# Kernel optimization log

Measured on AMD Instinct MI355X. Metric: run time of the kernel, lower is better.

The kernel has to match this reference:

```python
import jax, jax.numpy as jnp
import numpy as np

N = 30000      # nodes
E = 480000     # edges
H = 128        # hidden_nf
NQ = 7         # qubits
D = 2 ** NQ    # 128, quantum state dim == embedding_size
NL = 2         # block n_layers (QGCL layers)
QL = 2         # quantum circuit layers inside each QGCL
NORM = 100.0   # normalization_factor ('sum' aggregation)
NORM_CONST = 1.0


def _cnot_perm_indices(n):
    # Composed permutation for CNOT(0,1)...CNOT(n-2,n-1), CNOT(n-1,0).
    # PennyLane convention: wire 0 is the most significant bit.
    idx = np.arange(2 ** n)
    pairs = [(i, i + 1) for i in range(n - 1)] + [(n - 1, 0)]
    g = None
    for c, t in pairs:
        cb = (idx >> (n - 1 - c)) & 1
        f = idx ^ (cb << (n - 1 - t))  # flip target bit if control set (involution)
        g = f if g is None else g[f]
    return g

_CNOT_G = jnp.asarray(_cnot_perm_indices(NQ))


def _quantum_states(q_in, coeffs, A_re, A_im):
    """Vectorized VQC over all nodes. q_in [N,D] real -> [N,D] complex state."""
    norm = jnp.sqrt(jnp.sum(q_in ** 2, axis=1, keepdims=True) + 1e-12)
    s = (q_in / norm).astype(jnp.complex64)  # normalized initial state per node
    I = jnp.eye(D, dtype=jnp.complex64)
    for j in range(QL):
        # Cayley transform -> unitary
        A = (A_re[j] + 1j * A_im[j]).astype(jnp.complex64)
        A = A + A.conj().T
        q = (A - 1j * I) @ jnp.linalg.inv(A + 1j * I)
        # single-qubit layer: RY(b) @ RX(a) on every qubit -> kron power
        a, b = coeffs[j, 0].astype(jnp.complex64), coeffs[j, 1].astype(jnp.complex64)
        ca, sa = jnp.cos(a / 2), jnp.sin(a / 2)
        cb, sb = jnp.cos(b / 2), jnp.sin(b / 2)
        RX = jnp.stack([jnp.stack([ca, -1j * sa]), jnp.stack([-1j * sa, ca])])
        RY = jnp.stack([jnp.stack([cb, -sb]), jnp.stack([sb, cb])])
        G = RY @ RX
        Gk = G
        for _ in range(NQ - 1):
            Gk = jnp.kron(Gk, G)
        s = s @ q.T            # QubitUnitary
        s = s @ Gk.T           # RX/RY on all qubits
        s = s[:, _CNOT_G]      # CNOT ring (pure permutation)
    return s


def setup_inputs() -> dict:
    key = jax.random.key(0)
    ks = jax.random.split(key, 20)
    return {
        "h": jax.random.normal(ks[0], (N, H), jnp.float32),
        "x": jax.random.normal(ks[1], (N, 3), jnp.float32),
        "edge_index": jax.random.randint(ks[2], (2, E), 0, N, jnp.int32),
        "edge_attr": jax.random.normal(ks[3], (E, 1), jnp.float32),
        "e_w1": jax.random.normal(ks[4], (NL, 2 * H + 2, H), jnp.float32) * 0.05,
        "e_b1": jnp.zeros((NL, H), jnp.float32),
        "e_w2": jax.random.normal(ks[5], (NL, H, H), jnp.float32) * 0.05,
        "e_b2": jnp.zeros((NL, H), jnp.float32),
        "enc_w": jax.random.normal(ks[6], (NL, 2 * H, D), jnp.float32) * 0.05,
        "enc_b": jnp.zeros((NL, D), jnp.float32),
        "coeffs": jax.random.normal(ks[7], (NL, QL, 2), jnp.float32) * 0.1,
        "A_re": jax.random.normal(ks[8], (NL, QL, D, D), jnp.float32) * 0.01,
        "A_im": jax.random.normal(ks[9], (NL, QL, D, D), jnp.float32) * 0.01,
        "dec_w": jax.random.normal(ks[10], (NL, D, H), jnp.float32) * 0.05,
        "dec_b": jnp.zeros((NL, H), jnp.float32),
        "c_w1": jax.random.normal(ks[11], (2 * H + 2, H), jnp.float32) * 0.05,
        "c_b1": jnp.zeros((H,), jnp.float32),
        "c_w2": jax.random.normal(ks[12], (H, H), jnp.float32) * 0.05,
        "c_b2": jnp.zeros((H,), jnp.float32),
        "c_w3": jax.random.normal(ks[13], (H, 1), jnp.float32) * 0.001,  # xavier gain=0.001
    }


def reference(h, x, edge_index, edge_attr, e_w1, e_b1, e_w2, e_b2, enc_w, enc_b,
              coeffs, A_re, A_im, dec_w, dec_b, c_w1, c_b1, c_w2, c_b2, c_w3):
    row, col = edge_index[0], edge_index[1]
    # coord2diff
    diff = x[row] - x[col]
    radial = jnp.sum(diff ** 2, axis=1, keepdims=True)     # [E,1] (used as 'distances')
    coord_diff = diff / (jnp.sqrt(radial + 1e-8) + NORM_CONST)
    eattr = jnp.concatenate([radial, edge_attr], axis=1)   # [E,2]

    for l in range(NL):  # QGCL layers
        m = jnp.concatenate([h[row], h[col], eattr], axis=1)       # [E, 2H+2]
        m = jax.nn.silu(m @ e_w1[l] + e_b1[l])
        m = jax.nn.silu(m @ e_w2[l] + e_b2[l])                     # edge messages mij
        agg = jax.ops.segment_sum(m, row, num_segments=N) / NORM   # scatter-add
        q_in = jnp.concatenate([h, agg], axis=1) @ enc_w[l] + enc_b[l]
        # quantum part is detached in the original (torch .detach + re-tensor)
        qs = jax.lax.stop_gradient(
            _quantum_states(q_in, coeffs[l], A_re[l], A_im[l]))
        h = h + qs.real.astype(h.dtype) @ dec_w[l] + dec_b[l]

    # EquivariantUpdate (tanh=False)
    t = jnp.concatenate([h[row], h[col], eattr], axis=1)
    t = jax.nn.silu(t @ c_w1 + c_b1)
    t = jax.nn.silu(t @ c_w2 + c_b2)
    t = t @ c_w3                                                   # [E,1]
    trans = coord_diff * t
    x = x + jax.ops.segment_sum(trans, row, num_segments=N) / NORM
    return h, x
```

## Files before the change

### kernel.cpp

```cpp
#include <hip/hip_runtime.h>
#include <math.h>

#define N_NODES 30000
#define N_EDGES 480000
#define HDIM 128
#define EPB 64
#define NAS 264
#define MS 136
#define M2TS 72

typedef __attribute__((ext_vector_type(8))) short short8b;
typedef __attribute__((ext_vector_type(4))) float f32x4;

__device__ __forceinline__ float silu_f(float v) {
  return v / (1.0f + __expf(-v));
}

__device__ __forceinline__ unsigned short f2bf(float f) {
  unsigned int u = __float_as_uint(f);
  unsigned int r = u + 0x7fffu + ((u >> 16) & 1u);
  return (unsigned short)(r >> 16);
}

__device__ __forceinline__ unsigned int cvt_pk_bf16(float lo, float hi) {
  unsigned int r;
  asm("v_cvt_pk_bf16_f32 %0, %1, %2" : "=v"(r) : "v"(lo), "v"(hi));
  return r;
}

__device__ __forceinline__ ushort4 pk4(float4 v) {
  uint2 u;
  u.x = cvt_pk_bf16(v.x, v.y);
  u.y = cvt_pk_bf16(v.z, v.w);
  return *(ushort4*)&u;
}

__global__ void init_out_bf_kernel(const float* __restrict__ h,
                                   const float* __restrict__ x,
                                   const int* __restrict__ ei,
                                   float* __restrict__ out,
                                   int* __restrict__ cursor) {
  int idx = blockIdx.x * 256 + threadIdx.x;
  ((float4*)out)[idx] = ((const float4*)h)[idx];
  if (idx < N_NODES * 3 / 4) {
    ((float4*)(out + N_NODES * HDIM))[idx] = ((const float4*)x)[idx];
  }
  if (idx < N_EDGES) atomicAdd(&cursor[ei[idx]], 1);
}

__global__ __launch_bounds__(1024) void scan_kernel(int* __restrict__ cursor,
                                                    int* __restrict__ cstart) {
  __shared__ int sums[1024];
  const int tid = threadIdx.x;
  const int base = tid * 30;
  int local[30];
  int s = 0;
#pragma unroll
  for (int j = 0; j < 30; ++j) {
    int idx = base + j;
    int d = (idx < N_NODES) ? cursor[idx] : 0;
    local[j] = s;
    s += d;
  }
  sums[tid] = s;
  __syncthreads();
  for (int off = 1; off < 1024; off <<= 1) {
    int add = (tid >= off) ? sums[tid - off] : 0;
    __syncthreads();
    sums[tid] += add;
    __syncthreads();
  }
  int excl = (tid == 0) ? 0 : sums[tid - 1];
#pragma unroll
  for (int j = 0; j < 30; ++j) {
    int idx = base + j;
    if (idx < N_NODES) {
      int v = excl + local[j];
      cursor[idx] = v;
      cstart[idx] = v;
    }
  }
}

__global__ void prep_kernel(
    const int* __restrict__ ei, int* __restrict__ cursor,
    unsigned int* __restrict__ rcp, float2* __restrict__ era,
    const float* __restrict__ x, const float* __restrict__ ea,
    const float* __restrict__ e_w1, const float* __restrict__ e_w2,
    const float* __restrict__ enc_w, const float* __restrict__ c_w1,
    const float* __restrict__ c_w2,
    ushort* __restrict__ w1cs, ushort* __restrict__ w2cs,
    ushort* __restrict__ enccs, ushort* __restrict__ cw1cs,
    ushort* __restrict__ cw2cs,
    const float* __restrict__ A_re, const float* __restrict__ A_im,
    float2* __restrict__ X,
    const float* __restrict__ coeffs, float2* __restrict__ gkm,
    const float* __restrict__ outh, const float* __restrict__ b1l0,
    ushort* __restrict__ P) {
  __shared__ ushort Ht[EPB * MS];
  const int b = blockIdx.x, tid = threadIdx.x;
  if (b < 1875) {
    int e = b * 256 + tid;
    int r = ei[e];
    int c = ei[N_EDGES + e];
    int pos = atomicAdd(&cursor[r], 1);
    rcp[pos] = (unsigned int)r | ((unsigned int)c << 16);
    float dx = x[r * 3 + 0] - x[c * 3 + 0];
    float dy = x[r * 3 + 1] - x[c * 3 + 1];
    float dz = x[r * 3 + 2] - x[c * 3 + 2];
    era[pos] = make_float2(dx * dx + dy * dy + dz * dz, ea[e]);
  } else if (b < 2755) {
    int idx = (b - 1875) * 256 + tid;
    int ci = idx >> 12, rem = idx & 4095, kk = rem & 31;
    const float* W; ushort* dst; int Kreal, ktl;
    if (ci < 18) {
      int l = ci / 9; ktl = ci - l * 9;
      W = e_w1 + (size_t)l * 258 * HDIM; dst = w1cs + (size_t)l * 9 * 4096;
      Kreal = 258;
    } else if (ci < 26) {
      int c2 = ci - 18; int l = c2 >> 2; ktl = c2 & 3;
      W = e_w2 + (size_t)l * HDIM * HDIM; dst = w2cs + (size_t)l * 4 * 4096;
      Kreal = 128;
    } else if (ci < 42) {
      int c2 = ci - 26; int l = c2 >> 3; ktl = c2 & 7;
      W = enc_w + (size_t)l * 256 * HDIM; dst = enccs + (size_t)l * 8 * 4096;
      Kreal = 256;
    } else if (ci < 51) {
      ktl = ci - 42; W = c_w1; dst = cw1cs; Kreal = 258;
    } else {
      ktl = ci - 51; W = c_w2; dst = cw2cs; Kreal = 128;
    }
    int n = rem >> 5;
    int k = ktl * 32 + kk;
    float v = (k < Kreal) ? W[(size_t)k * HDIM + n] : 0.0f;
    dst[ktl * 4096 + rem] = f2bf(v);
  } else if (b < 3011) {
    int bb = b - 2755;
    int lj = bb >> 6;
    int idx = (bb & 63) * 256 + tid;
    int r = idx >> 7, c = idx & 127;
    const float* are = A_re + (size_t)lj * 16384;
    const float* aim = A_im + (size_t)lj * 16384;
    float re = are[r * 128 + c] + are[c * 128 + r];
    float im = aim[r * 128 + c] - aim[c * 128 + r];
    if (r == c) im -= 1.0f;
    X[(size_t)lj * 16384 + idx] = make_float2(re, im);
  } else if (b < 3267) {
    int bb = b - 3011;
    int lj = bb >> 6;
    float a = coeffs[lj * 2 + 0], bcf = coeffs[lj * 2 + 1];
    float ca = cosf(0.5f * a), sa = sinf(0.5f * a);
    float cb = cosf(0.5f * bcf), sb = sinf(0.5f * bcf);
    float2 G[2][2];
    G[0][0] = make_float2(cb * ca, sb * sa);
    G[0][1] = make_float2(-sb * ca, -cb * sa);
    G[1][0] = make_float2(sb * ca, -cb * sa);
    G[1][1] = make_float2(cb * ca, -sb * sa);
    int idx = (bb & 63) * 256 + tid;
    int r = idx >> 7, c = idx & 127;
    float2 acc = make_float2(1.f, 0.f);
#pragma unroll
    for (int bit = 6; bit >= 0; --bit) {
      float2 g = G[(r >> bit) & 1][(c >> bit) & 1];
      acc = make_float2(acc.x * g.x - acc.y * g.y, acc.x * g.y + acc.y * g.x);
    }
    gkm[(size_t)lj * 16384 + idx] = acc;
  } else {
    const int n0 = (b - 3267) * EPB;
    const int lane = tid & 63, wave = tid >> 6;
    const int lrow = lane & 15, lq = lane >> 4;
    {
      const int e = tid >> 2, jj = tid & 3;
      int node = n0 + e;
      if (node >= N_NODES) node = N_NODES - 1;
      const float4* s4 = (const float4*)(outh + (size_t)node * HDIM + jj * 32);
      ushort* dst = Ht + e * MS + jj * 32;
#pragma unroll
      for (int i = 0; i < 8; ++i) {
        ((ushort4*)dst)[i] = pk4(s4[i]);
      }
    }
    short8b wf[4][4];
    const int cs = (wave >> 1) * 4;
    const int nb = (wave & 1) * 64;
#pragma unroll
    for (int kt = 0; kt < 4; ++kt)
#pragma unroll
      for (int nt = 0; nt < 4; ++nt)
        wf[kt][nt] = *(const short8b*)(w1cs + (cs + kt) * 4096 + (nb + nt * 16 + lrow) * 32 + lq * 8);
    __syncthreads();

    f32x4 acc[4][4];
#pragma unroll
    for (int mt = 0; mt < 4; ++mt)
#pragma unroll
      for (int nt = 0; nt < 4; ++nt) acc[mt][nt] = (f32x4){0.f, 0.f, 0.f, 0.f};
#pragma unroll
    for (int kt = 0; kt < 4; ++kt) {
      short8b af[4];
#pragma unroll
      for (int mt = 0; mt < 4; ++mt)
        af[mt] = *(const short8b*)(Ht + (mt * 16 + lrow) * MS + kt * 32 + lq * 8);
#pragma unroll
      for (int mt = 0; mt < 4; ++mt)
#pragma unroll
        for (int nt = 0; nt < 4; ++nt)
          acc[mt][nt] = __builtin_amdgcn_mfma_f32_16x16x32_bf16(af[mt], wf[kt][nt], acc[mt][nt], 0, 0, 0);
    }
    const int cbase = wave * 64;
#pragma unroll
    for (int nt = 0; nt < 4; ++nt) {
      const int ccol = cbase + nt * 16 + lrow;
      const float bb2 = (ccol < 128) ? b1l0[ccol] : 0.f;
#pragma unroll
      for (int mt = 0; mt < 4; ++mt)
#pragma unroll
        for (int r = 0; r < 4; ++r) {
          const int node = n0 + mt * 16 + lq * 4 + r;
          if (node < N_NODES) P[(size_t)node * 256 + ccol] = f2bf(acc[mt][nt][r] + bb2);
        }
    }
  }
}

__global__ void ns_bx_kernel(const float* __restrict__ Are,
                             const float* __restrict__ Aim,
                             const float2* __restrict__ X,
                             float2* __restrict__ T) {
  int lj = blockIdx.y;
  int idx = blockIdx.x * 256 + threadIdx.x;
  int r = idx >> 7, c = idx & 127;
  const float* are = Are + (size_t)lj * 16384;
  const float* aim = Aim + (size_t)lj * 16384;
  const float2* x = X + (size_t)lj * 16384;
  float2 acc = make_float2(0.f, 0.f);
  for (int k = 0; k < 128; ++k) {
    float re = are[r * 128 + k] + are[k * 128 + r];
    float im = aim[r * 128 + k] - aim[k * 128 + r];
    if (k == r) im += 1.0f;
    float2 b = x[k * 128 + c];
    acc.x += re * b.x - im * b.y;
    acc.y += re * b.y + im * b.x;
  }
  T[(size_t)lj * 16384 + idx] = acc;
}

__global__ void ns_upd_kernel(const float2* __restrict__ X,
                              const float2* __restrict__ T,
                              float2* __restrict__ Xn) {
  int lj = blockIdx.y;
  int idx = blockIdx.x * 256 + threadIdx.x;
  int r = idx >> 7, c = idx & 127;
  const float2* x = X + (size_t)lj * 16384;
  const float2* t = T + (size_t)lj * 16384;
  float2 acc = make_float2(0.f, 0.f);
  for (int k = 0; k < 128; ++k) {
    float2 a = x[r * 128 + k];
    float2 b = t[k * 128 + c];
    acc.x += a.x * b.x - a.y * b.y;
    acc.y += a.x * b.y + a.y * b.x;
  }
  float2 xc = x[r * 128 + c];
  Xn[(size_t)lj * 16384 + idx] = make_float2(2.f * xc.x - acc.x, 2.f * xc.y - acc.y);
}

__global__ void qmat_kernel(const float* __restrict__ Are,
                            const float* __restrict__ Aim,
                            const float2* __restrict__ binvg,
                            float2* __restrict__ qm) {
  int lj = blockIdx.y;
  int idx = blockIdx.x * 256 + threadIdx.x;
  int r = idx >> 7, c = idx & 127;
  const float* are = Are + (size_t)lj * 16384;
  const float* aim = Aim + (size_t)lj * 16384;
  const float2* binv = binvg + (size_t)lj * 16384;
  float2 acc = make_float2(0.f, 0.f);
  for (int k = 0; k < 128; ++k) {
    float re = are[r * 128 + k] + are[k * 128 + r];
    float im = aim[r * 128 + k] - aim[k * 128 + r];
    if (k == r) im -= 1.0f;
    float2 b = binv[k * 128 + c];
    acc.x += re * b.x - im * b.y;
    acc.y += re * b.y + im * b.x;
  }
  qm[(size_t)lj * 16384 + idx] = acc;
}

__global__ void nj_kernel(const float2* __restrict__ qm,
                          const float2* __restrict__ gkm,
                          float2* __restrict__ njm) {
  int lj = blockIdx.y;
  int idx = blockIdx.x * 256 + threadIdx.x;
  int i = idx >> 7, c = idx & 127;
  int gc;
  {
    int v = c;
    const int cs[7] = {6, 5, 4, 3, 2, 1, 0};
    const int ts[7] = {0, 6, 5, 4, 3, 2, 1};
#pragma unroll
    for (int p = 0; p < 7; ++p) {
      int cb = (v >> (6 - cs[p])) & 1;
      v = v ^ (cb << (6 - ts[p]));
    }
    gc = v;
  }
  const float2* q = qm + (size_t)lj * 16384;
  const float2* gk = gkm + (size_t)lj * 16384;
  float2 acc = make_float2(0.f, 0.f);
  for (int k = 0; k < 128; ++k) {
    float2 qa = q[k * 128 + i];
    float2 gb = gk[gc * 128 + k];
    acc.x += qa.x * gb.x - qa.y * gb.y;
    acc.y += qa.x * gb.y + qa.y * gb.x;
  }
  njm[(size_t)lj * 16384 + idx] = acc;
}

__global__ void compose_kernel(const float2* __restrict__ njm,
                               float2* __restrict__ um) {
  int l = blockIdx.y;
  int idx = blockIdx.x * 256 + threadIdx.x;
  int i = idx >> 7, c = idx & 127;
  const float2* n0 = njm + (size_t)(l * 2 + 0) * 16384;
  const float2* n1 = njm + (size_t)(l * 2 + 1) * 16384;
  float2 acc = make_float2(0.f, 0.f);
  for (int k = 0; k < 128; ++k) {
    float2 a = n0[i * 128 + k];
    float2 b = n1[k * 128 + c];
    acc.x += a.x * b.x - a.y * b.y;
    acc.y += a.x * b.y + a.y * b.x;
  }
  um[(size_t)l * 16384 + idx] = acc;
}

__global__ void wqd_kernel(const float2* __restrict__ um,
                           const float* __restrict__ decw,
                           ushort* __restrict__ wqdcs) {
  int l = blockIdx.y;
  int idx = blockIdx.x * 256 + threadIdx.x;
  int i = idx >> 7, c = idx & 127;
  const float2* u = um + (size_t)l * 16384;
  const float* dw = decw + (size_t)l * 16384;
  float acc = 0.f;
  for (int k = 0; k < 128; ++k) acc += u[i * 128 + k].x * dw[k * 128 + c];
  wqdcs[(size_t)l * 4 * 4096 + (i >> 5) * 4096 + c * 32 + (i & 31)] = f2bf(acc);
}

__global__ __launch_bounds__(256, 4) void edge_mfma_kernel(
    const ushort* __restrict__ P, const unsigned int* __restrict__ rcp,
    const float2* __restrict__ era, const int* __restrict__ cstart,
    const float* __restrict__ wm,
    const ushort* __restrict__ w2cs, const float* __restrict__ b2,
    float* __restrict__ agg, float* __restrict__ headp) {
  __shared__ ushort buf[128 * M2TS];
  __shared__ int rows[EPB];
  __shared__ __align__(16) ushort segv[EPB];
  __shared__ int segnode[EPB];
  __shared__ int scont, snseg;
  ushort* m1 = buf;
  ushort* m2t = buf;

  const int tid = threadIdx.x;
  const int lane = tid & 63, wave = tid >> 6;
  const int lrow = lane & 15, lq = lane >> 4;
  const int wbase = wave * 32;
  const int woff0 = (wbase + lrow) * 32 + lq * 8;
  const int woff1 = (wbase + 16 + lrow) * 32 + lq * 8;
  const float b2v[2] = {b2[wbase + lrow], b2[wbase + 16 + lrow]};

  const int i0 = blockIdx.x * EPB;
  {
    const int e = tid >> 2, j = tid & 3;
    const unsigned int rcv = rcp[i0 + e];
    const int r = (int)(rcv & 0xFFFFu), c = (int)(rcv >> 16);
    if (j == 0) rows[e] = r;
    const float2 re2 = era[i0 + e];
    const float radial = re2.x, eav = re2.y;
    const uint4* pr = (const uint4*)(P + (size_t)r * 256 + j * 32);
    const uint4* pc = (const uint4*)(P + (size_t)c * 256 + 128 + j * 32);
    uint4 PR[4] = {pr[0], pr[1], pr[2], pr[3]};
    uint4 PC[4] = {pc[0], pc[1], pc[2], pc[3]};
#pragma unroll
    for (int q = 0; q < 4; ++q) {
      const int kb = j * 32 + q * 8;
      const uint ua[4] = {PR[q].x, PR[q].y, PR[q].z, PR[q].w};
      const uint ub[4] = {PC[q].x, PC[q].y, PC[q].z, PC[q].w};
      uint ow[4];
#pragma unroll
      for (int w = 0; w < 4; ++w) {
        const int k = kb + w * 2;
        float v0 = __uint_as_float(ua[w] << 16) + __uint_as_float(ub[w] << 16)
                 + radial * wm[k] + eav * wm[128 + k];
        float v1 = __uint_as_float(ua[w] & 0xffff0000u) + __uint_as_float(ub[w] & 0xffff0000u)
                 + radial * wm[k + 1] + eav * wm[129 + k];
        ow[w] = cvt_pk_bf16(silu_f(v0), silu_f(v1));
      }
      uint4 o; o.x = ow[0]; o.y = ow[1]; o.z = ow[2]; o.w = ow[3];
      *(uint4*)(m1 + e * MS + kb) = o;
    }
  }
  __syncthreads();

  f32x4 acc2[4][2];
#pragma unroll
  for (int mt = 0; mt < 4; ++mt)
#pragma unroll
    for (int nt = 0; nt < 2; ++nt) acc2[mt][nt] = (f32x4){0.f, 0.f, 0.f, 0.f};
  {
    short8b wcur0 = *(const short8b*)(w2cs + woff0);
    short8b wcur1 = *(const short8b*)(w2cs + woff1);
#pragma unroll
    for (int kt = 0; kt < 4; ++kt) {
      short8b wn0, wn1;
      if (kt < 3) {
        wn0 = *(const short8b*)(w2cs + (kt + 1) * 4096 + woff0);
        wn1 = *(const short8b*)(w2cs + (kt + 1) * 4096 + woff1);
      }
      short8b af[4];
#pragma unroll
      for (int mt = 0; mt < 4; ++mt)
        af[mt] = *(const short8b*)(m1 + (mt * 16 + lrow) * MS + kt * 32 + lq * 8);
#pragma unroll
      for (int mt = 0; mt < 4; ++mt) {
        acc2[mt][0] = __builtin_amdgcn_mfma_f32_16x16x32_bf16(af[mt], wcur0, acc2[mt][0], 0, 0, 0);
        acc2[mt][1] = __builtin_amdgcn_mfma_f32_16x16x32_bf16(af[mt], wcur1, acc2[mt][1], 0, 0, 0);
      }
      if (kt < 3) { wcur0 = wn0; wcur1 = wn1; }
    }
  }
  __syncthreads();

#pragma unroll
  for (int mt = 0; mt < 4; ++mt)
#pragma unroll
    for (int nt = 0; nt < 2; ++nt) {
      const int col = wbase + nt * 16 + lrow;
      uint2 u;
      u.x = cvt_pk_bf16(silu_f(acc2[mt][nt][0] + b2v[nt]),
                        silu_f(acc2[mt][nt][1] + b2v[nt]));
      u.y = cvt_pk_bf16(silu_f(acc2[mt][nt][2] + b2v[nt]),
                        silu_f(acc2[mt][nt][3] + b2v[nt]));
      *(uint2*)(m2t + col * M2TS + mt * 16 + lq * 4) = u;
    }
  if (wave == 0) {
    const int e = lane;
    const int re_ = rows[e];
    const bool leader = (e == 0) || (rows[e - 1] != re_);
    const unsigned long long mask = __ballot(leader);
    const int seg = (int)__popcll(mask & ((1ull << e) - 1ull));
    segv[e] = (ushort)seg;
    if (leader) segnode[seg] = re_;
    if (e == 0) {
      snseg = (int)__popcll(mask);
      scont = (cstart[re_] < i0) ? 1 : 0;
    }
  }
  __syncthreads();

  const int nseg = snseg, cont = scont;
  const int ntmax = (nseg + 15) >> 4;
  const short8b sv0 = *(const short8b*)(segv + lq * 8);
  const short8b sv1 = *(const short8b*)(segv + 32 + lq * 8);
  const int mtb = wave * 32;
  short8b afr[2][2];
#pragma unroll
  for (int mt = 0; mt < 2; ++mt) {
    const ushort* rp = m2t + (mtb + mt * 16 + lrow) * M2TS + lq * 8;
    afr[mt][0] = *(const short8b*)(rp);
    afr[mt][1] = *(const short8b*)(rp + 32);
  }
  for (int nt = 0; nt < ntmax; ++nt) {
    const int tgt = nt * 16 + lrow;
    uint p0[4], p1[4];
#pragma unroll
    for (int w = 0; w < 4; ++w) {
      p0[w] = (((int)(ushort)sv0[2 * w] == tgt) ? 0x3F80u : 0u)
            | (((int)(ushort)sv0[2 * w + 1] == tgt) ? 0x3F800000u : 0u);
      p1[w] = (((int)(ushort)sv1[2 * w] == tgt) ? 0x3F80u : 0u)
            | (((int)(ushort)sv1[2 * w + 1] == tgt) ? 0x3F800000u : 0u);
    }
    uint4 u0 = make_uint4(p0[0], p0[1], p0[2], p0[3]);
    uint4 u1 = make_uint4(p1[0], p1[1], p1[2], p1[3]);
    const short8b bf0 = *(const short8b*)&u0;
    const short8b bf1 = *(const short8b*)&u1;
    f32x4 r0 = (f32x4){0.f, 0.f, 0.f, 0.f};
    f32x4 r1 = (f32x4){0.f, 0.f, 0.f, 0.f};
    r0 = __builtin_amdgcn_mfma_f32_16x16x32_bf16(afr[0][0], bf0, r0, 0, 0, 0);
    r0 = __builtin_amdgcn_mfma_f32_16x16x32_bf16(afr[0][1], bf1, r0, 0, 0, 0);
    r1 = __builtin_amdgcn_mfma_f32_16x16x32_bf16(afr[1][0], bf0, r1, 0, 0, 0);
    r1 = __builtin_amdgcn_mfma_f32_16x16x32_bf16(afr[1][1], bf1, r1, 0, 0, 0);
    const int seg = tgt;
    if (seg < nseg) {
      const int node = segnode[seg];
      float* dst = (seg == 0 && cont) ? (headp + (size_t)blockIdx.x * HDIM)
                                      : (agg + (size_t)node * HDIM);
#pragma unroll
      for (int r = 0; r < 4; ++r) {
        dst[mtb + lq * 4 + r] = r0[r];
        dst[mtb + 16 + lq * 4 + r] = r1[r];
      }
    }
  }
}

__global__ __launch_bounds__(256, 2) void node_mfma_kernel(
    float* __restrict__ out_h, const float* __restrict__ agg,
    const int* __restrict__ cstart, const int* __restrict__ cend,
    const float* __restrict__ headp,
    const ushort* __restrict__ enccs, const float* __restrict__ encb,
    const ushort* __restrict__ wqdcs, const float* __restrict__ decb,
    const ushort* __restrict__ w1n, const float* __restrict__ b1n,
    ushort* __restrict__ Pout) {
  __shared__ ushort A[EPB * NAS];
  __shared__ ushort m1[EPB * MS];
  __shared__ float nbuf[4 * EPB];
  const int tid = threadIdx.x;
  const int n0 = blockIdx.x * EPB;

  const int lane = tid & 63, wave = tid >> 6;
  const int lrow = lane & 15, lq = lane >> 4;
  const int wbase = wave * 32;

  short8b wef[8][2], wqf[4][2];
#pragma unroll
  for (int kt = 0; kt < 8; ++kt)
#pragma unroll
    for (int nt = 0; nt < 2; ++nt)
      wef[kt][nt] = *(const short8b*)(enccs + kt * 4096 + (wbase + nt * 16 + lrow) * 32 + lq * 8);
#pragma unroll
  for (int kt = 0; kt < 4; ++kt)
#pragma unroll
    for (int nt = 0; nt < 2; ++nt)
      wqf[kt][nt] = *(const short8b*)(wqdcs + kt * 4096 + (wbase + nt * 16 + lrow) * 32 + lq * 8);
  const float ebv[2] = {encb[wbase + lrow], encb[wbase + 16 + lrow]};
  const float dbv[2] = {decb[wbase + lrow], decb[wbase + 16 + lrow]};

  {
    const int e = tid >> 2, j = tid & 3;
    int node = n0 + e;
    if (node >= N_NODES) node = N_NODES - 1;
    if (j < 2) {
      const float4* s4 = (const float4*)(out_h + (size_t)node * HDIM + j * 64);
      ushort* dst = A + e * NAS + j * 64;
#pragma unroll
      for (int i = 0; i < 16; ++i) {
        ((ushort4*)dst)[i] = pk4(s4[i]);
      }
    } else {
      const int s = cstart[node], en = cend[node];
      const bool hasAgg = en > s;
      const float4* a4 = (const float4*)(agg + (size_t)node * HDIM + (j - 2) * 64);
      const int bb0 = (s >> 6) + 1;
      const int bb1 = hasAgg ? ((en - 1) >> 6) : 0;
      ushort* dst = A + e * NAS + 128 + (j - 2) * 64;
#pragma unroll
      for (int i = 0; i < 16; ++i) {
        float4 v = hasAgg ? a4[i] : make_float4(0.f, 0.f, 0.f, 0.f);
        for (int bb = bb0; bb <= bb1; ++bb) {
          float4 hv = *(const float4*)(headp + (size_t)bb * HDIM + (j - 2) * 64 + i * 4);
          v.x += hv.x; v.y += hv.y; v.z += hv.z; v.w += hv.w;
        }
        float4 sv = make_float4(v.x * 0.01f, v.y * 0.01f, v.z * 0.01f, v.w * 0.01f);
        ((ushort4*)dst)[i] = pk4(sv);
      }
    }
  }
  __syncthreads();

  f32x4 acc[4][2];
#pragma unroll
  for (int mt = 0; mt < 4; ++mt)
#pragma unroll
    for (int nt = 0; nt < 2; ++nt) acc[mt][nt] = (f32x4){0.f, 0.f, 0.f, 0.f};
#pragma unroll
  for (int kt = 0; kt < 8; ++kt) {
    short8b af[4];
#pragma unroll
    for (int mt = 0; mt < 4; ++mt)
      af[mt] = *(const short8b*)(A + (mt * 16 + lrow) * NAS + kt * 32 + lq * 8);
#pragma unroll
    for (int mt = 0; mt < 4; ++mt)
#pragma unroll
      for (int nt = 0; nt < 2; ++nt)
        acc[mt][nt] = __builtin_amdgcn_mfma_f32_16x16x32_bf16(af[mt], wef[kt][nt], acc[mt][nt], 0, 0, 0);
  }
#pragma unroll
  for (int mt = 0; mt < 4; ++mt) {
    float ssp[4] = {0.f, 0.f, 0.f, 0.f};
#pragma unroll
    for (int nt = 0; nt < 2; ++nt)
#pragma unroll
      for (int r = 0; r < 4; ++r) {
        acc[mt][nt][r] += ebv[nt];
        ssp[r] += acc[mt][nt][r] * acc[mt][nt][r];
      }
#pragma unroll
    for (int m = 1; m < 16; m <<= 1)
#pragma unroll
      for (int r = 0; r < 4; ++r) ssp[r] += __shfl_xor(ssp[r], m, 64);
    if (lrow == 0) {
#pragma unroll
      for (int r = 0; r < 4; ++r)
        nbuf[wave * EPB + mt * 16 + lq * 4 + r] = ssp[r];
    }
  }
  __syncthreads();
#pragma unroll
  for (int mt = 0; mt < 4; ++mt)
#pragma unroll
    for (int r = 0; r < 4; ++r) {
      const int row = mt * 16 + lq * 4 + r;
      float sum = nbuf[row] + nbuf[EPB + row] + nbuf[2 * EPB + row] + nbuf[3 * EPB + row];
      float inv = 1.0f / sqrtf(sum + 1e-12f);
#pragma unroll
      for (int nt = 0; nt < 2; ++nt)
        m1[row * MS + wbase + nt * 16 + lrow] = f2bf(acc[mt][nt][r] * inv);
    }
  __syncthreads();

  f32x4 acc2[4][2];
#pragma unroll
  for (int mt = 0; mt < 4; ++mt)
#pragma unroll
    for (int nt = 0; nt < 2; ++nt) acc2[mt][nt] = (f32x4){0.f, 0.f, 0.f, 0.f};
#pragma unroll
  for (int kt = 0; kt < 4; ++kt) {
    short8b af[4];
#pragma unroll
    for (int mt = 0; mt < 4; ++mt)
      af[mt] = *(const short8b*)(m1 + (mt * 16 + lrow) * MS + kt * 32 + lq * 8);
#pragma unroll
    for (int mt = 0; mt < 4; ++mt)
#pragma unroll
      for (int nt = 0; nt < 2; ++nt)
        acc2[mt][nt] = __builtin_amdgcn_mfma_f32_16x16x32_bf16(af[mt], wqf[kt][nt], acc2[mt][nt], 0, 0, 0);
  }
  __syncthreads();

#pragma unroll
  for (int mt = 0; mt < 4; ++mt)
#pragma unroll
    for (int nt = 0; nt < 2; ++nt) {
      const int n = wbase + nt * 16 + lrow;
#pragma unroll
      for (int r = 0; r < 4; ++r) {
        const int node = n0 + mt * 16 + lq * 4 + r;
        float hn = 0.f;
        if (node < N_NODES) {
          size_t off = (size_t)node * HDIM + n;
          hn = out_h[off] + acc2[mt][nt][r] + dbv[nt];
          out_h[off] = hn;
        }
        m1[(mt * 16 + lq * 4 + r) * MS + n] = f2bf(hn);
      }
    }
  __syncthreads();

  short8b wfp[4][4];
  const int csn = (wave >> 1) * 4;
  const int nbw = (wave & 1) * 64;
#pragma unroll
  for (int kt = 0; kt < 4; ++kt)
#pragma unroll
    for (int nt = 0; nt < 4; ++nt)
      wfp[kt][nt] = *(const short8b*)(w1n + (csn + kt) * 4096 + (nbw + nt * 16 + lrow) * 32 + lq * 8);
  f32x4 pacc[4][4];
#pragma unroll
  for (int mt = 0; mt < 4; ++mt)
#pragma unroll
    for (int nt = 0; nt < 4; ++nt) pacc[mt][nt] = (f32x4){0.f, 0.f, 0.f, 0.f};
#pragma unroll
  for (int kt = 0; kt < 4; ++kt) {
    short8b af[4];
#pragma unroll
    for (int mt = 0; mt < 4; ++mt)
      af[mt] = *(const short8b*)(m1 + (mt * 16 + lrow) * MS + kt * 32 + lq * 8);
#pragma unroll
    for (int mt = 0; mt < 4; ++mt)
#pragma unroll
      for (int nt = 0; nt < 4; ++nt)
        pacc[mt][nt] = __builtin_amdgcn_mfma_f32_16x16x32_bf16(af[mt], wfp[kt][nt], pacc[mt][nt], 0, 0, 0);
  }
  const int cbase = wave * 64;
#pragma unroll
  for (int nt = 0; nt < 4; ++nt) {
    const int ccol = cbase + nt * 16 + lrow;
    const float bb2 = (ccol < 128) ? b1n[ccol] : 0.f;
#pragma unroll
    for (int mt = 0; mt < 4; ++mt)
#pragma unroll
      for (int r = 0; r < 4; ++r) {
        const int node = n0 + mt * 16 + lq * 4 + r;
        if (node < N_NODES) Pout[(size_t)node * 256 + ccol] = f2bf(pacc[mt][nt][r] + bb2);
      }
  }
}

__global__ __launch_bounds__(256, 4) void coord_mfma_kernel(
    const ushort* __restrict__ P, const unsigned int* __restrict__ rcp,
    const float2* __restrict__ era, const float* __restrict__ x,
    const float* __restrict__ wm,
    const ushort* __restrict__ w2cs, const float* __restrict__ b2,
    const float* __restrict__ w3, float* __restrict__ xout) {
  __shared__ ushort m1[EPB * MS];
  __shared__ int rows[EPB];
  __shared__ float pbuf[4 * EPB];
  __shared__ float tv[EPB];
  __shared__ float dxs[EPB], dys[EPB], dzs[EPB], ses[EPB];

  const int tid = threadIdx.x;
  const int lane = tid & 63, wave = tid >> 6;
  const int lrow = lane & 15, lq = lane >> 4;
  const int wbase = wave * 32;
  const int woff0 = (wbase + lrow) * 32 + lq * 8;
  const int woff1 = (wbase + 16 + lrow) * 32 + lq * 8;

  const float b2v[2] = {b2[wbase + lrow], b2[wbase + 16 + lrow]};
  const float w3v[2] = {w3[wbase + lrow], w3[wbase + 16 + lrow]};

  const int i0 = blockIdx.x * EPB;
  {
    const int e = tid >> 2, j = tid & 3;
    const unsigned int rcv = rcp[i0 + e];
    const int r = (int)(rcv & 0xFFFFu), c = (int)(rcv >> 16);
    if (j == 0) rows[e] = r;
    const float2 re2 = era[i0 + e];
    const float radial = re2.x, eav = re2.y;
    const uint4* pr = (const uint4*)(P + (size_t)r * 256 + j * 32);
    const uint4* pc = (const uint4*)(P + (size_t)c * 256 + 128 + j * 32);
    uint4 PR[4] = {pr[0], pr[1], pr[2], pr[3]};
    uint4 PC[4] = {pc[0], pc[1], pc[2], pc[3]};
    if (j == 3) {
      float dx = x[r * 3 + 0] - x[c * 3 + 0];
      float dy = x[r * 3 + 1] - x[c * 3 + 1];
      float dz = x[r * 3 + 2] - x[c * 3 + 2];
      dxs[e] = dx; dys[e] = dy; dzs[e] = dz;
      ses[e] = 1.0f / (sqrtf(radial + 1e-8f) + 1.0f);
    }
#pragma unroll
    for (int q = 0; q < 4; ++q) {
      const int kb = j * 32 + q * 8;
      const uint ua[4] = {PR[q].x, PR[q].y, PR[q].z, PR[q].w};
      const uint ub[4] = {PC[q].x, PC[q].y, PC[q].z, PC[q].w};
      uint ow[4];
#pragma unroll
      for (int w = 0; w < 4; ++w) {
        const int k = kb + w * 2;
        float v0 = __uint_as_float(ua[w] << 16) + __uint_as_float(ub[w] << 16)
                 + radial * wm[k] + eav * wm[128 + k];
        float v1 = __uint_as_float(ua[w] & 0xffff0000u) + __uint_as_float(ub[w] & 0xffff0000u)
                 + radial * wm[k + 1] + eav * wm[129 + k];
        ow[w] = cvt_pk_bf16(silu_f(v0), silu_f(v1));
      }
      uint4 o; o.x = ow[0]; o.y = ow[1]; o.z = ow[2]; o.w = ow[3];
      *(uint4*)(m1 + e * MS + kb) = o;
    }
  }
  __syncthreads();

  f32x4 acc2[4][2];
#pragma unroll
  for (int mt = 0; mt < 4; ++mt)
#pragma unroll
    for (int nt = 0; nt < 2; ++nt) acc2[mt][nt] = (f32x4){0.f, 0.f, 0.f, 0.f};
  {
    short8b wcur0 = *(const short8b*)(w2cs + woff0);
    short8b wcur1 = *(const short8b*)(w2cs + woff1);
#pragma unroll
    for (int kt = 0; kt < 4; ++kt) {
      short8b wn0, wn1;
      if (kt < 3) {
        wn0 = *(const short8b*)(w2cs + (kt + 1) * 4096 + woff0);
        wn1 = *(const short8b*)(w2cs + (kt + 1) * 4096 + woff1);
      }
      short8b af[4];
#pragma unroll
      for (int mt = 0; mt < 4; ++mt)
        af[mt] = *(const short8b*)(m1 + (mt * 16 + lrow) * MS + kt * 32 + lq * 8);
#pragma unroll
      for (int mt = 0; mt < 4; ++mt) {
        acc2[mt][0] = __builtin_amdgcn_mfma_f32_16x16x32_bf16(af[mt], wcur0, acc2[mt][0], 0, 0, 0);
        acc2[mt][1] = __builtin_amdgcn_mfma_f32_16x16x32_bf16(af[mt], wcur1, acc2[mt][1], 0, 0, 0);
      }
      if (kt < 3) { wcur0 = wn0; wcur1 = wn1; }
    }
  }
#pragma unroll
  for (int mt = 0; mt < 4; ++mt) {
    float p[4] = {0.f, 0.f, 0.f, 0.f};
#pragma unroll
    for (int nt = 0; nt < 2; ++nt)
#pragma unroll
      for (int r = 0; r < 4; ++r)
        p[r] += silu_f(acc2[mt][nt][r] + b2v[nt]) * w3v[nt];
#pragma unroll
    for (int m = 1; m < 16; m <<= 1)
#pragma unroll
      for (int r = 0; r < 4; ++r) p[r] += __shfl_xor(p[r], m, 64);
    if (lrow == 0) {
#pragma unroll
      for (int r = 0; r < 4; ++r)
        pbuf[wave * EPB + mt * 16 + lq * 4 + r] = p[r];
    }
  }
  __syncthreads();
  if (tid < EPB) {
    tv[tid] = (pbuf[tid] + pbuf[EPB + tid] + pbuf[2 * EPB + tid] + pbuf[3 * EPB + tid])
              * 0.01f * ses[tid];
  }
  __syncthreads();
  if (tid < EPB) {
    const int e = tid;
    const int r_e = rows[e];
    const bool leader = (e == 0) || (rows[e - 1] != r_e);
    if (leader) {
      float sx = 0.f, sy = 0.f, sz = 0.f;
      int f = e;
      do {
        float t = tv[f];
        sx += dxs[f] * t; sy += dys[f] * t; sz += dzs[f] * t;
        ++f;
      } while (f < EPB && rows[f] == r_e);
      atomicAdd(&xout[r_e * 3 + 0], sx);
      atomicAdd(&xout[r_e * 3 + 1], sy);
      atomicAdd(&xout[r_e * 3 + 2], sz);
    }
  }
}

extern "C" void kernel_launch(void* const* d_in, const int* in_sizes, int n_in,
                              void* d_out, int out_size, void* d_ws, size_t ws_size,
                              hipStream_t stream) {
  const float* h     = (const float*)d_in[0];
  const float* x     = (const float*)d_in[1];
  const int*   ei    = (const int*)d_in[2];
  const float* ea    = (const float*)d_in[3];
  const float* e_w1  = (const float*)d_in[4];
  const float* e_b1  = (const float*)d_in[5];
  const float* e_w2  = (const float*)d_in[6];
  const float* e_b2  = (const float*)d_in[7];
  const float* enc_w = (const float*)d_in[8];
  const float* enc_b = (const float*)d_in[9];
  const float* coeffs= (const float*)d_in[10];
  const float* A_re  = (const float*)d_in[11];
  const float* A_im  = (const float*)d_in[12];
  const float* dec_w = (const float*)d_in[13];
  const float* dec_b = (const float*)d_in[14];
  const float* c_w1  = (const float*)d_in[15];
  const float* c_b1  = (const float*)d_in[16];
  const float* c_w2  = (const float*)d_in[17];
  const float* c_b2  = (const float*)d_in[18];
  const float* c_w3  = (const float*)d_in[19];

  float* out = (float*)d_out;
  float* ws  = (float*)d_ws;

  float*        agg    = ws;
  float2*       xa     = (float2*)(ws + 3840000);
  float2*       xb     = (float2*)(ws + 3971072);
  float2*       xt     = (float2*)(ws + 4102144);
  float2*       qm     = (float2*)(ws + 4233216);
  float2*       gkm    = (float2*)(ws + 4364288);
  float2*       njm    = (float2*)(ws + 4495360);
  float2*       um     = (float2*)(ws + 4626432);
  int*          cursor = (int*)(ws + 4724864);
  int*          cstart = (int*)(ws + 4754864);
  unsigned int* rcp    = (unsigned int*)(ws + 4784864);
  float2*       era    = (float2*)(ws + 5264864);
  float*        headp  = ws + 6224864;
  ushort*       w1cs   = (ushort*)(ws + 7184864);
  ushort*       w2cs   = (ushort*)(ws + 7221728);
  ushort*       cw1cs  = (ushort*)(ws + 7238112);
  ushort*       cw2cs  = (ushort*)(ws + 7256544);
  ushort*       enccs  = (ushort*)(ws + 7264736);
  ushort*       wqdcs  = (ushort*)(ws + 7297504);
  ushort*       Pbuf   = (ushort*)(ws + 7313888);

  hipMemsetAsync(cursor, 0, N_NODES * sizeof(int), stream);
  init_out_bf_kernel<<<3750, 256, 0, stream>>>(h, x, ei, out, cursor);
  scan_kernel<<<1, 1024, 0, stream>>>(cursor, cstart);

  prep_kernel<<<3736, 256, 0, stream>>>(ei, cursor, rcp, era, x, ea,
                                        e_w1, e_w2, enc_w, c_w1, c_w2,
                                        w1cs, w2cs, enccs, cw1cs, cw2cs,
                                        A_re, A_im, xa, coeffs, gkm,
                                        out, e_b1, Pbuf);

  float2* cur = xa;
  float2* nxt = xb;
  for (int it = 0; it < 2; ++it) {
    ns_bx_kernel<<<dim3(64, 4), 256, 0, stream>>>(A_re, A_im, cur, xt);
    ns_upd_kernel<<<dim3(64, 4), 256, 0, stream>>>(cur, xt, nxt);
    float2* tmp = cur; cur = nxt; nxt = tmp;
  }
  qmat_kernel<<<dim3(64, 4), 256, 0, stream>>>(A_re, A_im, cur, qm);
  nj_kernel<<<dim3(64, 4), 256, 0, stream>>>(qm, gkm, njm);
  compose_kernel<<<dim3(64, 2), 256, 0, stream>>>(njm, um);
  wqd_kernel<<<dim3(64, 2), 256, 0, stream>>>(um, dec_w, wqdcs);

  const int NB = (N_NODES + EPB - 1) / EPB;

  for (int l = 0; l < 2; ++l) {
    edge_mfma_kernel<<<N_EDGES / EPB, 256, 0, stream>>>(
        Pbuf, rcp, era, cstart,
        e_w1 + (size_t)l * 258 * HDIM + 256 * HDIM,
        w2cs + (size_t)l * 4 * 4096, e_b2 + l * HDIM, agg, headp);
    node_mfma_kernel<<<NB, 256, 0, stream>>>(
        out, agg, cstart, cursor, headp,
        enccs + (size_t)l * 8 * 4096, enc_b + l * HDIM,
        wqdcs + (size_t)l * 4 * 4096, dec_b + l * HDIM,
        (l == 0) ? (w1cs + (size_t)9 * 4096) : cw1cs,
        (l == 0) ? (e_b1 + HDIM) : c_b1,
        Pbuf);
  }

  coord_mfma_kernel<<<N_EDGES / EPB, 256, 0, stream>>>(
      Pbuf, rcp, era, x, c_w1 + 256 * HDIM, cw2cs, c_b2, c_w3,
      out + (size_t)N_NODES * HDIM);
}
```

Baseline: 661.8 us.

## Halve edge tile to 32 edges with 128-thread blocks in edge and coord kernels

Edge-block size for the edge-message and coordinate kernels drops from 64 to 32 edges, and the blocks shrink to two waves. Each wave now computes 64 output columns over all 32 edges, and the segment-reduction MFMA is reworked for a single 32-edge K-slice. Head-partial indexing in the node kernel is updated to the new block size, and the workspace offsets move to fit the larger headp buffer. The aim is more resident blocks and less LDS per block, at the cost of twice as many blocks, more boundary partials, and reloading the weight fragments per block.

```diff
diff --git a/kernel.cpp b/kernel.cpp
--- a/kernel.cpp
+++ b/kernel.cpp
@@ -5,9 +5,10 @@
 #define N_EDGES 480000
 #define HDIM 128
 #define EPB 64
+#define EB 32
 #define NAS 264
 #define MS 136
-#define M2TS 72
+#define M2TS 36
 
 typedef __attribute__((ext_vector_type(8))) short short8b;
 typedef __attribute__((ext_vector_type(4))) float f32x4;
@@ -346,16 +347,16 @@
   wqdcs[(size_t)l * 4 * 4096 + (i >> 5) * 4096 + c * 32 + (i & 31)] = f2bf(acc);
 }
 
-__global__ __launch_bounds__(256, 4) void edge_mfma_kernel(
+__global__ __launch_bounds__(128, 8) void edge_mfma_kernel(
     const ushort* __restrict__ P, const unsigned int* __restrict__ rcp,
     const float2* __restrict__ era, const int* __restrict__ cstart,
     const float* __restrict__ wm,
     const ushort* __restrict__ w2cs, const float* __restrict__ b2,
     float* __restrict__ agg, float* __restrict__ headp) {
   __shared__ ushort buf[128 * M2TS];
-  __shared__ int rows[EPB];
-  __shared__ __align__(16) ushort segv[EPB];
-  __shared__ int segnode[EPB];
+  __shared__ int rows[EB];
+  __shared__ __align__(16) ushort segv[EB];
+  __shared__ int segnode[EB];
   __shared__ int scont, snseg;
   ushort* m1 = buf;
   ushort* m2t = buf;
@@ -363,12 +364,11 @@
   const int tid = threadIdx.x;
   const int lane = tid & 63, wave = tid >> 6;
   const int lrow = lane & 15, lq = lane >> 4;
-  const int wbase = wave * 32;
-  const int woff0 = (wbase + lrow) * 32 + lq * 8;
-  const int woff1 = (wbase + 16 + lrow) * 32 + lq * 8;
-  const float b2v[2] = {b2[wbase + lrow], b2[wbase + 16 + lrow]};
-
-  const int i0 = blockIdx.x * EPB;
+  const int cb = wave * 64;
+  const float b2v[4] = {b2[cb + lrow], b2[cb + 16 + lrow],
+                        b2[cb + 32 + lrow], b2[cb + 48 + lrow]};
+
+  const int i0 = blockIdx.x * EB;
   {
     const int e = tid >> 2, j = tid & 3;
     const unsigned int rcv = rcp[i0 + e];
@@ -401,40 +401,34 @@
   }
   __syncthreads();
 
-  f32x4 acc2[4][2];
-#pragma unroll
-  for (int mt = 0; mt < 4; ++mt)
-#pragma unroll
-    for (int nt = 0; nt < 2; ++nt) acc2[mt][nt] = (f32x4){0.f, 0.f, 0.f, 0.f};
-  {
-    short8b wcur0 = *(const short8b*)(w2cs + woff0);
-    short8b wcur1 = *(const short8b*)(w2cs + woff1);
-#pragma unroll
-    for (int kt = 0; kt < 4; ++kt) {
-      short8b wn0, wn1;
-      if (kt < 3) {
-        wn0 = *(const short8b*)(w2cs + (kt + 1) * 4096 + woff0);
-        wn1 = *(const short8b*)(w2cs + (kt + 1) * 4096 + woff1);
-      }
-      short8b af[4];
-#pragma unroll
-      for (int mt = 0; mt < 4; ++mt)
-        af[mt] = *(const short8b*)(m1 + (mt * 16 + lrow) * MS + kt * 32 + lq * 8);
-#pragma unroll
-      for (int mt = 0; mt < 4; ++mt) {
-        acc2[mt][0] = __builtin_amdgcn_mfma_f32_16x16x32_bf16(af[mt], wcur0, acc2[mt][0], 0, 0, 0);
-        acc2[mt][1] = __builtin_amdgcn_mfma_f32_16x16x32_bf16(af[mt], wcur1, acc2[mt][1], 0, 0, 0);
-      }
-      if (kt < 3) { wcur0 = wn0; wcur1 = wn1; }
-    }
-  }
-  __syncthreads();
-
-#pragma unroll
-  for (int mt = 0; mt < 4; ++mt)
-#pragma unroll
-    for (int nt = 0; nt < 2; ++nt) {
-      const int col = wbase + nt * 16 + lrow;
+  f32x4 acc2[2][4];
+#pragma unroll
+  for (int mt = 0; mt < 2; ++mt)
+#pragma unroll
+    for (int nt = 0; nt < 4; ++nt) acc2[mt][nt] = (f32x4){0.f, 0.f, 0.f, 0.f};
+#pragma unroll
+  for (int kt = 0; kt < 4; ++kt) {
+    short8b wf[4];
+#pragma unroll
+    for (int nt = 0; nt < 4; ++nt)
+      wf[nt] = *(const short8b*)(w2cs + kt * 4096 + (cb + nt * 16 + lrow) * 32 + lq * 8);
+    short8b af[2];
+#pragma unroll
+    for (int mt = 0; mt < 2; ++mt)
+      af[mt] = *(const short8b*)(m1 + (mt * 16 + lrow) * MS + kt * 32 + lq * 8);
+#pragma unroll
+    for (int mt = 0; mt < 2; ++mt)
+#pragma unroll
+      for (int nt = 0; nt < 4; ++nt)
+        acc2[mt][nt] = __builtin_amdgcn_mfma_f32_16x16x32_bf16(af[mt], wf[nt], acc2[mt][nt], 0, 0, 0);
+  }
+  __syncthreads();
+
+#pragma unroll
+  for (int mt = 0; mt < 2; ++mt)
+#pragma unroll
+    for (int nt = 0; nt < 4; ++nt) {
+      const int col = cb + nt * 16 + lrow;
       uint2 u;
       u.x = cvt_pk_bf16(silu_f(acc2[mt][nt][0] + b2v[nt]),
                         silu_f(acc2[mt][nt][1] + b2v[nt]));
@@ -444,12 +438,15 @@
     }
   if (wave == 0) {
     const int e = lane;
-    const int re_ = rows[e];
-    const bool leader = (e == 0) || (rows[e - 1] != re_);
+    const bool valid = e < EB;
+    const int re_ = rows[valid ? e : (EB - 1)];
+    const bool leader = valid && (e == 0 || rows[e - 1] != re_);
     const unsigned long long mask = __ballot(leader);
-    const int seg = (int)__popcll(mask & ((1ull << e) - 1ull));
-    segv[e] = (ushort)seg;
-    if (leader) segnode[seg] = re_;
+    if (valid) {
+      const int seg = (int)__popcll(mask & ((1ull << e) - 1ull));
+      segv[e] = (ushort)seg;
+      if (leader) segnode[seg] = re_;
+    }
     if (e == 0) {
       snseg = (int)__popcll(mask);
       scont = (cstart[re_] < i0) ? 1 : 0;
@@ -459,46 +456,37 @@
 
   const int nseg = snseg, cont = scont;
   const int ntmax = (nseg + 15) >> 4;
-  const short8b sv0 = *(const short8b*)(segv + lq * 8);
-  const short8b sv1 = *(const short8b*)(segv + 32 + lq * 8);
-  const int mtb = wave * 32;
-  short8b afr[2][2];
-#pragma unroll
-  for (int mt = 0; mt < 2; ++mt) {
-    const ushort* rp = m2t + (mtb + mt * 16 + lrow) * M2TS + lq * 8;
-    afr[mt][0] = *(const short8b*)(rp);
-    afr[mt][1] = *(const short8b*)(rp + 32);
-  }
+  const short8b sv = *(const short8b*)(segv + lq * 8);
+  short8b afr[4];
+#pragma unroll
+  for (int mi = 0; mi < 4; ++mi)
+    afr[mi] = *(const short8b*)(m2t + (cb + mi * 16 + lrow) * M2TS + lq * 8);
   for (int nt = 0; nt < ntmax; ++nt) {
     const int tgt = nt * 16 + lrow;
-    uint p0[4], p1[4];
+    uint p[4];
 #pragma unroll
     for (int w = 0; w < 4; ++w) {
-      p0[w] = (((int)(ushort)sv0[2 * w] == tgt) ? 0x3F80u : 0u)
-            | (((int)(ushort)sv0[2 * w + 1] == tgt) ? 0x3F800000u : 0u);
-      p1[w] = (((int)(ushort)sv1[2 * w] == tgt) ? 0x3F80u : 0u)
-            | (((int)(ushort)sv1[2 * w + 1] == tgt) ? 0x3F800000u : 0u);
-    }
-    uint4 u0 = make_uint4(p0[0], p0[1], p0[2], p0[3]);
-    uint4 u1 = make_uint4(p1[0], p1[1], p1[2], p1[3]);
-    const short8b bf0 = *(const short8b*)&u0;
-    const short8b bf1 = *(const short8b*)&u1;
-    f32x4 r0 = (f32x4){0.f, 0.f, 0.f, 0.f};
-    f32x4 r1 = (f32x4){0.f, 0.f, 0.f, 0.f};
-    r0 = __builtin_amdgcn_mfma_f32_16x16x32_bf16(afr[0][0], bf0, r0, 0, 0, 0);
-    r0 = __builtin_amdgcn_mfma_f32_16x16x32_bf16(afr[0][1], bf1, r0, 0, 0, 0);
-    r1 = __builtin_amdgcn_mfma_f32_16x16x32_bf16(afr[1][0], bf0, r1, 0, 0, 0);
-    r1 = __builtin_amdgcn_mfma_f32_16x16x32_bf16(afr[1][1], bf1, r1, 0, 0, 0);
+      p[w] = (((int)(ushort)sv[2 * w] == tgt) ? 0x3F80u : 0u)
+           | (((int)(ushort)sv[2 * w + 1] == tgt) ? 0x3F800000u : 0u);
+    }
+    uint4 u0 = make_uint4(p[0], p[1], p[2], p[3]);
+    const short8b bf = *(const short8b*)&u0;
+    f32x4 racc[4];
+#pragma unroll
+    for (int mi = 0; mi < 4; ++mi) {
+      racc[mi] = (f32x4){0.f, 0.f, 0.f, 0.f};
+      racc[mi] = __builtin_amdgcn_mfma_f32_16x16x32_bf16(afr[mi], bf, racc[mi], 0, 0, 0);
+    }
     const int seg = tgt;
     if (seg < nseg) {
       const int node = segnode[seg];
       float* dst = (seg == 0 && cont) ? (headp + (size_t)blockIdx.x * HDIM)
                                       : (agg + (size_t)node * HDIM);
 #pragma unroll
-      for (int r = 0; r < 4; ++r) {
-        dst[mtb + lq * 4 + r] = r0[r];
-        dst[mtb + 16 + lq * 4 + r] = r1[r];
-      }
+      for (int mi = 0; mi < 4; ++mi)
+#pragma unroll
+        for (int r = 0; r < 4; ++r)
+          dst[cb + mi * 16 + lq * 4 + r] = racc[mi][r];
     }
   }
 }
@@ -550,8 +538,8 @@
       const int s = cstart[node], en = cend[node];
       const bool hasAgg = en > s;
       const float4* a4 = (const float4*)(agg + (size_t)node * HDIM + (j - 2) * 64);
-      const int bb0 = (s >> 6) + 1;
-      const int bb1 = hasAgg ? ((en - 1) >> 6) : 0;
+      const int bb0 = (s >> 5) + 1;
+      const int bb1 = hasAgg ? ((en - 1) >> 5) : 0;
       ushort* dst = A + e * NAS + 128 + (j - 2) * 64;
 #pragma unroll
       for (int i = 0; i < 16; ++i) {
@@ -696,29 +684,29 @@
   }
 }
 
-__global__ __launch_bounds__(256, 4) void coord_mfma_kernel(
+__global__ __launch_bounds__(128, 8) void coord_mfma_kernel(
     const ushort* __restrict__ P, const unsigned int* __restrict__ rcp,
     const float2* __restrict__ era, const float* __restrict__ x,
     const float* __restrict__ wm,
     const ushort* __restrict__ w2cs, const float* __restrict__ b2,
     const float* __restrict__ w3, float* __restrict__ xout) {
-  __shared__ ushort m1[EPB * MS];
-  __shared__ int rows[EPB];
-  __shared__ float pbuf[4 * EPB];
-  __shared__ float tv[EPB];
-  __shared__ float dxs[EPB], dys[EPB], dzs[EPB], ses[EPB];
+  __shared__ ushort m1[EB * MS];
+  __shared__ int rows[EB];
+  __shared__ float pbuf[2 * EB];
+  __shared__ float tv[EB];
+  __shared__ float dxs[EB], dys[EB], dzs[EB], ses[EB];
 
   const int tid = threadIdx.x;
   const int lane = tid & 63, wave = tid >> 6;
   const int lrow = lane & 15, lq = lane >> 4;
-  const int wbase = wave * 32;
-  const int woff0 = (wbase + lrow) * 32 + lq * 8;
-  const int woff1 = (wbase + 16 + lrow) * 32 + lq * 8;
-
-  const float b2v[2] = {b2[wbase + lrow], b2[wbase + 16 + lrow]};
-  const float w3v[2] = {w3[wbase + lrow], w3[wbase + 16 + lrow]};
-
-  const int i0 = blockIdx.x * EPB;
+  const int cb = wave * 64;
+
+  const float b2v[4] = {b2[cb + lrow], b2[cb + 16 + lrow],
+                        b2[cb + 32 + lrow], b2[cb + 48 + lrow]};
+  const float w3v[4] = {w3[cb + lrow], w3[cb + 16 + lrow],
+                        w3[cb + 32 + lrow], w3[cb + 48 + lrow]};
+
+  const int i0 = blockIdx.x * EB;
   {
     const int e = tid >> 2, j = tid & 3;
     const unsigned int rcv = rcp[i0 + e];
@@ -758,38 +746,33 @@
   }
   __syncthreads();
 
-  f32x4 acc2[4][2];
-#pragma unroll
-  for (int mt = 0; mt < 4; ++mt)
-#pragma unroll
-    for (int nt = 0; nt < 2; ++nt) acc2[mt][nt] = (f32x4){0.f, 0.f, 0.f, 0.f};
-  {
-    short8b wcur0 = *(const short8b*)(w2cs + woff0);
-    short8b wcur1 = *(const short8b*)(w2cs + woff1);
-#pragma unroll
-    for (int kt = 0; kt < 4; ++kt) {
-      short8b wn0, wn1;
-      if (kt < 3) {
-        wn0 = *(const short8b*)(w2cs + (kt + 1) * 4096 + woff0);
-        wn1 = *(const short8b*)(w2cs + (kt + 1) * 4096 + woff1);
-      }
-      short8b af[4];
-#pragma unroll
-      for (int mt = 0; mt < 4; ++mt)
-        af[mt] = *(const short8b*)(m1 + (mt * 16 + lrow) * MS + kt * 32 + lq * 8);
-#pragma unroll
-      for (int mt = 0; mt < 4; ++mt) {
-        acc2[mt][0] = __builtin_amdgcn_mfma_f32_16x16x32_bf16(af[mt], wcur0, acc2[mt][0], 0, 0, 0);
-        acc2[mt][1] = __builtin_amdgcn_mfma_f32_16x16x32_bf16(af[mt], wcur1, acc2[mt][1], 0, 0, 0);
-      }
-      if (kt < 3) { wcur0 = wn0; wcur1 = wn1; }
-    }
-  }
-#pragma unroll
-  for (int mt = 0; mt < 4; ++mt) {
+  f32x4 acc2[2][4];
+#pragma unroll
+  for (int mt = 0; mt < 2; ++mt)
+#pragma unroll
+    for (int nt = 0; nt < 4; ++nt) acc2[mt][nt] = (f32x4){0.f, 0.f, 0.f, 0.f};
+#pragma unroll
+  for (int kt = 0; kt < 4; ++kt) {
+    short8b wf[4];
+#pragma unroll
+    for (int nt = 0; nt < 4; ++nt)
+      wf[nt] = *(const short8b*)(w2cs + kt * 4096 + (cb + nt * 16 + lrow) * 32 + lq * 8);
+    short8b af[2];
+#pragma unroll
+    for (int mt = 0; mt < 2; ++mt)
+      af[mt] = *(const short8b*)(m1 + (mt * 16 + lrow) * MS + kt * 32 + lq * 8);
+#pragma unroll
+    for (int mt = 0; mt < 2; ++mt)
+#pragma unroll
+      for (int nt = 0; nt < 4; ++nt)
+        acc2[mt][nt] = __builtin_amdgcn_mfma_f32_16x16x32_bf16(af[mt], wf[nt], acc2[mt][nt], 0, 0, 0);
+  }
+
+#pragma unroll
+  for (int mt = 0; mt < 2; ++mt) {
     float p[4] = {0.f, 0.f, 0.f, 0.f};
 #pragma unroll
-    for (int nt = 0; nt < 2; ++nt)
+    for (int nt = 0; nt < 4; ++nt)
 #pragma unroll
       for (int r = 0; r < 4; ++r)
         p[r] += silu_f(acc2[mt][nt][r] + b2v[nt]) * w3v[nt];
@@ -800,16 +783,15 @@
     if (lrow == 0) {
 #pragma unroll
       for (int r = 0; r < 4; ++r)
-        pbuf[wave * EPB + mt * 16 + lq * 4 + r] = p[r];
-    }
-  }
-  __syncthreads();
-  if (tid < EPB) {
-    tv[tid] = (pbuf[tid] + pbuf[EPB + tid] + pbuf[2 * EPB + tid] + pbuf[3 * EPB + tid])
-              * 0.01f * ses[tid];
-  }
-  __syncthreads();
-  if (tid < EPB) {
+        pbuf[wave * EB + mt * 16 + lq * 4 + r] = p[r];
+    }
+  }
+  __syncthreads();
+  if (tid < EB) {
+    tv[tid] = (pbuf[tid] + pbuf[EB + tid]) * 0.01f * ses[tid];
+  }
+  __syncthreads();
+  if (tid < EB) {
     const int e = tid;
     const int r_e = rows[e];
     const bool leader = (e == 0) || (rows[e - 1] != r_e);
@@ -820,7 +802,7 @@
         float t = tv[f];
         sx += dxs[f] * t; sy += dys[f] * t; sz += dzs[f] * t;
         ++f;
-      } while (f < EPB && rows[f] == r_e);
+      } while (f < EB && rows[f] == r_e);
       atomicAdd(&xout[r_e * 3 + 0], sx);
       atomicAdd(&xout[r_e * 3 + 1], sy);
       atomicAdd(&xout[r_e * 3 + 2], sz);
@@ -868,13 +850,13 @@
   unsigned int* rcp    = (unsigned int*)(ws + 4784864);
   float2*       era    = (float2*)(ws + 5264864);
   float*        headp  = ws + 6224864;
-  ushort*       w1cs   = (ushort*)(ws + 7184864);
-  ushort*       w2cs   = (ushort*)(ws + 7221728);
-  ushort*       cw1cs  = (ushort*)(ws + 7238112);
-  ushort*       cw2cs  = (ushort*)(ws + 7256544);
-  ushort*       enccs  = (ushort*)(ws + 7264736);
-  ushort*       wqdcs  = (ushort*)(ws + 7297504);
-  ushort*       Pbuf   = (ushort*)(ws + 7313888);
+  ushort*       w1cs   = (ushort*)(ws + 8144864);
+  ushort*       w2cs   = (ushort*)(ws + 8181728);
+  ushort*       cw1cs  = (ushort*)(ws + 8198112);
+  ushort*       cw2cs  = (ushort*)(ws + 8216544);
+  ushort*       enccs  = (ushort*)(ws + 8224736);
+  ushort*       wqdcs  = (ushort*)(ws + 8257504);
+  ushort*       Pbuf   = (ushort*)(ws + 8273888);
 
   hipMemsetAsync(cursor, 0, N_NODES * sizeof(int), stream);
   init_out_bf_kernel<<<3750, 256, 0, stream>>>(h, x, ei, out, cursor);
@@ -901,7 +883,7 @@
   const int NB = (N_NODES + EPB - 1) / EPB;
 
   for (int l = 0; l < 2; ++l) {
-    edge_mfma_kernel<<<N_EDGES / EPB, 256, 0, stream>>>(
+    edge_mfma_kernel<<<N_EDGES / EB, 128, 0, stream>>>(
         Pbuf, rcp, era, cstart,
         e_w1 + (size_t)l * 258 * HDIM + 256 * HDIM,
         w2cs + (size_t)l * 4 * 4096, e_b2 + l * HDIM, agg, headp);
@@ -914,7 +896,7 @@
         Pbuf);
   }
 
-  coord_mfma_kernel<<<N_EDGES / EPB, 256, 0, stream>>>(
+  coord_mfma_kernel<<<N_EDGES / EB, 128, 0, stream>>>(
       Pbuf, rcp, era, x, c_w1 + 256 * HDIM, cw2cs, c_b2, c_w3,
       out + (size_t)N_NODES * HDIM);
 }
```

Result: slower. 784.9 us (+18.6%).
